# Performance work log

Measured on AMD Instinct MI355X. Metric: run time of the kernel, lower is better.

The kernel has to match this reference:

```python
import jax, jax.numpy as jnp
import numpy as np

B, C, L, E = 2048, 128, 16, 10      # atoms, channels, num_ell=(lmax+1)^2, elements
P3, P2, P1 = 23, 4, 1               # num CG paths per correlation order
U_DENSITY = 0.15                    # CG-like U tensors are highly sparse


def _sparse_u(key, shape):
    k1, k2 = jax.random.split(key)
    vals = jax.random.normal(k1, shape, dtype=jnp.float32)
    mask = jax.random.uniform(k2, shape) < U_DENSITY
    return jnp.where(mask, vals, 0.0)


def setup_inputs() -> dict:
    key = jax.random.key(0)
    ks = jax.random.split(key, 8)
    x = jax.random.normal(ks[0], (B, C, L), dtype=jnp.float32)
    y = jax.random.uniform(ks[1], (B, E), dtype=jnp.float32)  # element attrs
    U3 = _sparse_u(ks[2], (L, L, L, P3))
    U2 = _sparse_u(ks[3], (L, L, P2))
    U1 = _sparse_u(ks[4], (L, P1))
    W3 = jax.random.normal(ks[5], (E, P3, C), dtype=jnp.float32) / P3
    W2 = jax.random.normal(ks[6], (E, P2, C), dtype=jnp.float32) / P2
    W1 = jax.random.normal(ks[7], (E, P1, C), dtype=jnp.float32) / P1
    return {"x": x, "y": y, "U3": U3, "U2": U2, "U1": U1,
            "W3": W3, "W2": W2, "W1": W1}


def reference(x, y, U3, U2, U1, W3, W2, W1):
    # nu=3 main contraction: 'wxik,ekc,bci,be->bcwx'
    out = jnp.einsum('wxik,ekc,bci,be->bcwx', U3, W3, x, y, optimize='optimal')  # [B,C,L,L]
    # nu=2: weighting then feature contraction
    c2 = jnp.einsum('wxk,ekc,be->bcwx', U2, W2, y, optimize='optimal') + out
    out = jnp.einsum('bcwi,bci->bcw', c2, x)                                     # [B,C,L]
    # nu=1
    c1 = jnp.einsum('wk,ekc,be->bcw', U1, W1, y, optimize='optimal') + out
    out = jnp.einsum('bci,bci->bc', c1, x)                                       # [B,C]
    return out.reshape(out.shape[0], -1)
```

## Files before the change

kernel.cpp:

```cpp
#include <hip/hip_runtime.h>
#include <hip/hip_bf16.h>

typedef __attribute__((ext_vector_type(8))) short short8;
typedef __attribute__((ext_vector_type(4))) float f32x4;

#define LL 16
#define NP3 23
#define NE 10
#define NC 128
#define KI 24
#define NSTEPS 12
#define MT 64
#define THREADS 1024
#define NWAVES 16
#define ZCOLS 392

__global__ void build_B(const float* __restrict__ U3, const float* __restrict__ U2,
                        __hip_bfloat16* __restrict__ Bf) {
    int s    = blockIdx.x >> 4;
    int n16  = blockIdx.x & 15;
    int lane = threadIdx.x;
    int ar   = lane & 15, kg = lane >> 4;
    int n    = n16 * 16 + ar;
    __hip_bfloat16 vals[8];
#pragma unroll
    for (int j = 0; j < 8; ++j) {
        int kk = s * 32 + kg * 8 + j;
        int i  = kk / KI, k = kk - i * KI;
        float v;
        if (k < NP3)      v = U3[((size_t)n * LL + i) * NP3 + k];
        else if (i < 4)   v = U2[n * 4 + i];
        else              v = 0.f;
        vals[j] = __float2bfloat16(v);
    }
    *reinterpret_cast<short8*>(Bf + ((size_t)blockIdx.x * 64 + lane) * 8) =
        *reinterpret_cast<short8*>(vals);
}

__global__ __launch_bounds__(THREADS, 8)
void contract_k(const float* __restrict__ x, const float* __restrict__ y,
                const float* __restrict__ W3, const float* __restrict__ W2,
                const float* __restrict__ W1, const float* __restrict__ U1,
                const __hip_bfloat16* __restrict__ Bf, float* __restrict__ out) {
    __shared__ __align__(16) __hip_bfloat16 Zt[MT][ZCOLS];
    __shared__ float xs[MT][16];
    __shared__ float wys[MT][28];
    float (*part)[NWAVES] = reinterpret_cast<float (*)[NWAVES]>(&Zt[0][0]);

    const int tid = threadIdx.x;
    const int m0  = blockIdx.x * MT;
    const int b   = m0 >> 7;
    const int c0  = m0 & (NC - 1);

    xs[tid >> 4][tid & 15] = x[(size_t)m0 * LL + tid];

    float yv[NE];
#pragma unroll
    for (int e = 0; e < NE; ++e) yv[e] = y[(size_t)b * NE + e];

    for (int u = tid; u < 28 * MT; u += THREADS) {
        int idx = u >> 6, r = u & 63;
        int c = c0 + r;
        float s = 0.f;
        if (idx < NP3) {
#pragma unroll
            for (int e = 0; e < NE; ++e) s += yv[e] * W3[(e * NP3 + idx) * NC + c];
        } else if (idx < 27) {
            int k2 = idx - NP3;
#pragma unroll
            for (int e = 0; e < NE; ++e) s += yv[e] * W2[(e * 4 + k2) * NC + c];
        } else {
#pragma unroll
            for (int e = 0; e < NE; ++e) s += yv[e] * W1[e * NC + c];
        }
        wys[r][idx] = s;
    }
    __syncthreads();

    {
        int r = tid >> 4, i = tid & 15;
        float xi = xs[r][i];
        __hip_bfloat162 pk[12];
#pragma unroll
        for (int kp = 0; kp < 12; ++kp) {
            float a  = xi * wys[r][2 * kp];
            float bb = (kp < 11) ? xi * wys[r][2 * kp + 1]
                                 : ((i < 4) ? wys[r][NP3 + i] : 0.f);
            pk[kp].x = __float2bfloat16(a);
            pk[kp].y = __float2bfloat16(bb);
        }
        const short8* pv = reinterpret_cast<const short8*>(pk);
        short8* dst = reinterpret_cast<short8*>(&Zt[r][i * KI]);
        dst[0] = pv[0]; dst[1] = pv[1]; dst[2] = pv[2];
    }
    __syncthreads();

    const int lane = tid & 63;
    const int nw   = tid >> 6;
    const int ar   = lane & 15;
    const int kg   = lane >> 4;
    f32x4 acc[4];
#pragma unroll
    for (int mt = 0; mt < 4; ++mt) acc[mt] = f32x4{0.f, 0.f, 0.f, 0.f};

    const short8* Bw = reinterpret_cast<const short8*>(Bf) + (size_t)nw * 64 + lane;
    short8 bcur = Bw[0];
#pragma unroll
    for (int s = 0; s < NSTEPS; ++s) {
        short8 bnxt = bcur;
        if (s + 1 < NSTEPS) bnxt = Bw[(size_t)(s + 1) * 1024];
#pragma unroll
        for (int mt = 0; mt < 4; ++mt) {
            short8 a = *reinterpret_cast<const short8*>(&Zt[mt * 16 + ar][s * 32 + kg * 8]);
            acc[mt] = __builtin_amdgcn_mfma_f32_16x16x32_bf16(a, bcur, acc[mt], 0, 0, 0);
        }
        bcur = bnxt;
    }
    __syncthreads();

#pragma unroll
    for (int mt = 0; mt < 4; ++mt) {
#pragma unroll
        for (int q = 0; q < 4; ++q) {
            int row = mt * 16 + kg * 4 + q;
            float sl = acc[mt][q] * xs[row][ar];
            sl += __shfl_xor(sl, 1);
            sl += __shfl_xor(sl, 2);
            sl += __shfl_xor(sl, 4);
            sl += __shfl_xor(sl, 8);
            if (ar == 0) part[row][nw] = xs[row][nw] * sl;
        }
    }
    __syncthreads();

    if (tid < MT) {
        int r = tid;
        float s = 0.f;
#pragma unroll
        for (int w = 0; w < NWAVES; ++w) s += part[r][w];
        float du = 0.f;
#pragma unroll
        for (int w = 0; w < LL; ++w) du += U1[w] * xs[r][w];
        out[m0 + r] = s + wys[r][27] * du;
    }
}

extern "C" void kernel_launch(void* const* d_in, const int* in_sizes, int n_in,
                              void* d_out, int out_size, void* d_ws, size_t ws_size,
                              hipStream_t stream) {
    const float* x  = (const float*)d_in[0];
    const float* y  = (const float*)d_in[1];
    const float* U3 = (const float*)d_in[2];
    const float* U2 = (const float*)d_in[3];
    const float* U1 = (const float*)d_in[4];
    const float* W3 = (const float*)d_in[5];
    const float* W2 = (const float*)d_in[6];
    const float* W1 = (const float*)d_in[7];
    __hip_bfloat16* Bf = (__hip_bfloat16*)d_ws;

    build_B<<<NSTEPS * 16, 64, 0, stream>>>(U3, U2, Bf);
    contract_k<<<4096, THREADS, 0, stream>>>(x, y, W3, W2, W1, U1, Bf, (float*)d_out);
}
```

Before: 126.9 us.

## Keep A operand in registers and use 32x32x16 MFMA with per-atom blocks

```diff
diff --git a/kernel.cpp b/kernel.cpp
--- a/kernel.cpp
+++ b/kernel.cpp
@@ -2,146 +2,169 @@
 #include <hip/hip_bf16.h>
 
 typedef __attribute__((ext_vector_type(8))) short short8;
-typedef __attribute__((ext_vector_type(4))) float f32x4;
+typedef __attribute__((ext_vector_type(16))) float f32x16;
 
 #define LL 16
 #define NP3 23
 #define NE 10
 #define NC 128
 #define KI 24
-#define NSTEPS 12
-#define MT 64
-#define THREADS 1024
-#define NWAVES 16
-#define ZCOLS 392
+#define NSK 24
+#define NT 8
+#define MB 128
+#define THREADS 256
+
+static __device__ __forceinline__ short f2bs(float f) {
+    __hip_bfloat16 h = __float2bfloat16(f);
+    short s;
+    __builtin_memcpy(&s, &h, 2);
+    return s;
+}
 
 __global__ void build_B(const float* __restrict__ U3, const float* __restrict__ U2,
                         __hip_bfloat16* __restrict__ Bf) {
-    int s    = blockIdx.x >> 4;
-    int n16  = blockIdx.x & 15;
+    int g = blockIdx.x;
+    int t = g / NSK, s = g % NSK;
     int lane = threadIdx.x;
-    int ar   = lane & 15, kg = lane >> 4;
-    int n    = n16 * 16 + ar;
-    __hip_bfloat16 vals[8];
+    int col  = t * 32 + (lane & 31);
+    int hi   = lane >> 5;
+    short8 v;
 #pragma unroll
     for (int j = 0; j < 8; ++j) {
-        int kk = s * 32 + kg * 8 + j;
-        int i  = kk / KI, k = kk - i * KI;
-        float v;
-        if (k < NP3)      v = U3[((size_t)n * LL + i) * NP3 + k];
-        else if (i < 4)   v = U2[n * 4 + i];
-        else              v = 0.f;
-        vals[j] = __float2bfloat16(v);
+        int K = s * 16 + hi * 8 + j;
+        int i = K / KI, kk = K - i * KI;
+        float f;
+        if (kk < NP3)    f = U3[((size_t)col * LL + i) * NP3 + kk];
+        else if (i < 4)  f = U2[col * 4 + i];
+        else             f = 0.f;
+        v[j] = f2bs(f);
     }
-    *reinterpret_cast<short8*>(Bf + ((size_t)blockIdx.x * 64 + lane) * 8) =
-        *reinterpret_cast<short8*>(vals);
+    *reinterpret_cast<short8*>(Bf + ((size_t)g * 64 + lane) * 8) = v;
 }
 
-__global__ __launch_bounds__(THREADS, 8)
+#define BUILD_A(HIOFF)                                                        \
+    _Pragma("unroll")                                                         \
+    for (int s = 0; s < NSK; ++s) {                                           \
+        short8 av;                                                            \
+        _Pragma("unroll")                                                     \
+        for (int j = 0; j < 8; ++j) {                                         \
+            const int K  = s * 16 + (HIOFF) + j;                              \
+            const int i  = K / KI;                                            \
+            const int kk = K - i * KI;                                        \
+            float f = (kk < NP3) ? xr[i] * wr[kk]                             \
+                                 : ((i < 4) ? w2r[i] : 0.f);                  \
+            av[j] = f2bs(f);                                                  \
+        }                                                                     \
+        A[s] = av;                                                            \
+    }
+
+__global__ __launch_bounds__(THREADS, 2)
 void contract_k(const float* __restrict__ x, const float* __restrict__ y,
                 const float* __restrict__ W3, const float* __restrict__ W2,
                 const float* __restrict__ W1, const float* __restrict__ U1,
                 const __hip_bfloat16* __restrict__ Bf, float* __restrict__ out) {
-    __shared__ __align__(16) __hip_bfloat16 Zt[MT][ZCOLS];
-    __shared__ float xs[MT][16];
-    __shared__ float wys[MT][28];
-    float (*part)[NWAVES] = reinterpret_cast<float (*)[NWAVES]>(&Zt[0][0]);
+    __shared__ float xs[MB][17];
+    __shared__ float wys[MB][29];
 
     const int tid = threadIdx.x;
-    const int m0  = blockIdx.x * MT;
-    const int b   = m0 >> 7;
-    const int c0  = m0 & (NC - 1);
+    const int m0  = blockIdx.x * MB;
+    const int b   = blockIdx.x;
 
-    xs[tid >> 4][tid & 15] = x[(size_t)m0 * LL + tid];
+    for (int idx = tid; idx < MB * LL; idx += THREADS)
+        xs[idx >> 4][idx & 15] = x[(size_t)m0 * LL + idx];
+    __syncthreads();
 
     float yv[NE];
 #pragma unroll
     for (int e = 0; e < NE; ++e) yv[e] = y[(size_t)b * NE + e];
 
-    for (int u = tid; u < 28 * MT; u += THREADS) {
-        int idx = u >> 6, r = u & 63;
-        int c = c0 + r;
+    for (int u = tid; u < 29 * MB; u += THREADS) {
+        int idx = u >> 7, r = u & (MB - 1);
         float s = 0.f;
         if (idx < NP3) {
 #pragma unroll
-            for (int e = 0; e < NE; ++e) s += yv[e] * W3[(e * NP3 + idx) * NC + c];
+            for (int e = 0; e < NE; ++e) s += yv[e] * W3[(e * NP3 + idx) * NC + r];
         } else if (idx < 27) {
-            int k2 = idx - NP3;
 #pragma unroll
-            for (int e = 0; e < NE; ++e) s += yv[e] * W2[(e * 4 + k2) * NC + c];
+            for (int e = 0; e < NE; ++e) s += yv[e] * W2[(e * 4 + (idx - NP3)) * NC + r];
+        } else if (idx == 27) {
+#pragma unroll
+            for (int e = 0; e < NE; ++e) s += yv[e] * W1[e * NC + r];
         } else {
 #pragma unroll
-            for (int e = 0; e < NE; ++e) s += yv[e] * W1[e * NC + c];
+            for (int w = 0; w < LL; ++w) s += U1[w] * xs[r][w];
         }
         wys[r][idx] = s;
     }
     __syncthreads();
 
+    const int lane = tid & 63;
+    const int wb   = tid >> 6;
+    const int l31  = lane & 31;
+    const int hi   = lane >> 5;
+    const int bsel = l31 >> 4;
+    const int arow = wb * 32 + l31;
+
+    short8 A[NSK];
     {
-        int r = tid >> 4, i = tid & 15;
-        float xi = xs[r][i];
-        __hip_bfloat162 pk[12];
+        float xr[LL], wr[NP3], w2r[4];
 #pragma unroll
-        for (int kp = 0; kp < 12; ++kp) {
-            float a  = xi * wys[r][2 * kp];
-            float bb = (kp < 11) ? xi * wys[r][2 * kp + 1]
-                                 : ((i < 4) ? wys[r][NP3 + i] : 0.f);
-            pk[kp].x = __float2bfloat16(a);
-            pk[kp].y = __float2bfloat16(bb);
-        }
-        const short8* pv = reinterpret_cast<const short8*>(pk);
-        short8* dst = reinterpret_cast<short8*>(&Zt[r][i * KI]);
-        dst[0] = pv[0]; dst[1] = pv[1]; dst[2] = pv[2];
+        for (int i = 0; i < LL; ++i) xr[i] = xs[arow][i];
+#pragma unroll
+        for (int k = 0; k < NP3; ++k) wr[k] = wys[arow][k];
+#pragma unroll
+        for (int i = 0; i < 4; ++i) w2r[i] = wys[arow][NP3 + i];
+        if (hi == 0) { BUILD_A(0) } else { BUILD_A(8) }
     }
-    __syncthreads();
 
-    const int lane = tid & 63;
-    const int nw   = tid >> 6;
-    const int ar   = lane & 15;
-    const int kg   = lane >> 4;
-    f32x4 acc[4];
+    float xx[16];
 #pragma unroll
-    for (int mt = 0; mt < 4; ++mt) acc[mt] = f32x4{0.f, 0.f, 0.f, 0.f};
+    for (int q = 0; q < 16; ++q) {
+        int rowq = (wb << 5) + (q & 3) + ((q >> 2) << 3) + (hi << 2);
+        xx[q] = xs[rowq][lane & 15];
+    }
 
-    const short8* Bw = reinterpret_cast<const short8*>(Bf) + (size_t)nw * 64 + lane;
-    short8 bcur = Bw[0];
+    const short8* Bv = reinterpret_cast<const short8*>(Bf);
+    short8 bf[6];
 #pragma unroll
-    for (int s = 0; s < NSTEPS; ++s) {
-        short8 bnxt = bcur;
-        if (s + 1 < NSTEPS) bnxt = Bw[(size_t)(s + 1) * 1024];
+    for (int j = 0; j < 6; ++j) bf[j] = Bv[(size_t)j * 64 + lane];
+
+    float acc_out[16];
 #pragma unroll
-        for (int mt = 0; mt < 4; ++mt) {
-            short8 a = *reinterpret_cast<const short8*>(&Zt[mt * 16 + ar][s * 32 + kg * 8]);
-            acc[mt] = __builtin_amdgcn_mfma_f32_16x16x32_bf16(a, bcur, acc[mt], 0, 0, 0);
-        }
-        bcur = bnxt;
-    }
-    __syncthreads();
+    for (int q = 0; q < 16; ++q) acc_out[q] = 0.f;
 
 #pragma unroll
-    for (int mt = 0; mt < 4; ++mt) {
+    for (int t = 0; t < NT; ++t) {
+        f32x16 acc;
 #pragma unroll
-        for (int q = 0; q < 4; ++q) {
-            int row = mt * 16 + kg * 4 + q;
-            float sl = acc[mt][q] * xs[row][ar];
-            sl += __shfl_xor(sl, 1);
-            sl += __shfl_xor(sl, 2);
-            sl += __shfl_xor(sl, 4);
-            sl += __shfl_xor(sl, 8);
-            if (ar == 0) part[row][nw] = xs[row][nw] * sl;
+        for (int q = 0; q < 16; ++q) acc[q] = 0.f;
+#pragma unroll
+        for (int s = 0; s < NSK; ++s) {
+            const int g = t * NSK + s;
+            acc = __builtin_amdgcn_mfma_f32_32x32x16_bf16(A[s], bf[g % 6], acc, 0, 0, 0);
+            if (g + 6 < NT * NSK)
+                bf[g % 6] = Bv[(size_t)(g + 6) * 64 + lane];
+        }
+#pragma unroll
+        for (int q = 0; q < 16; ++q) {
+            int rowq = (wb << 5) + (q & 3) + ((q >> 2) << 3) + (hi << 2);
+            float xw = xs[rowq][2 * t + bsel];
+            acc_out[q] += acc[q] * xx[q] * xw;
         }
     }
-    __syncthreads();
 
-    if (tid < MT) {
-        int r = tid;
-        float s = 0.f;
 #pragma unroll
-        for (int w = 0; w < NWAVES; ++w) s += part[r][w];
-        float du = 0.f;
-#pragma unroll
-        for (int w = 0; w < LL; ++w) du += U1[w] * xs[r][w];
-        out[m0 + r] = s + wys[r][27] * du;
+    for (int q = 0; q < 16; ++q) {
+        float v = acc_out[q];
+        v += __shfl_xor(v, 1);
+        v += __shfl_xor(v, 2);
+        v += __shfl_xor(v, 4);
+        v += __shfl_xor(v, 8);
+        v += __shfl_xor(v, 16);
+        if (l31 == 0) {
+            int rowq = (wb << 5) + (q & 3) + ((q >> 2) << 3) + (hi << 2);
+            out[m0 + rowq] = v + wys[rowq][27] * wys[rowq][28];
+        }
     }
 }
 
@@ -158,6 +181,6 @@
     const float* W1 = (const float*)d_in[7];
     __hip_bfloat16* Bf = (__hip_bfloat16*)d_ws;
 
-    build_B<<<NSTEPS * 16, 64, 0, stream>>>(U3, U2, Bf);
-    contract_k<<<4096, THREADS, 0, stream>>>(x, y, W3, W2, W1, U1, Bf, (float*)d_out);
+    build_B<<<NT * NSK, 64, 0, stream>>>(U3, U2, Bf);
+    contract_k<<<2048, THREADS, 0, stream>>>(x, y, W3, W2, W1, U1, Bf, (float*)d_out);
 }
```

Result: faster. 116.0 us (-8.6%).
